# Performance work log

Measured on AMD Instinct MI355X. Metric: run time of the kernel, lower is better.

Reference implementation:

```python
import jax, jax.numpy as jnp
import numpy as np

PAD = 0
B, M, N, E = 32, 512, 512, 768
NEG_INF = 1e12
SCALE = np.float32(np.sqrt(768.0))


def submult(a, b):
    d = a - b
    return jnp.concatenate([a, b, d, a * b, d * d], axis=-1)


def setup_inputs() -> dict:
    key = jax.random.key(0)
    ks = jax.random.split(key, 8)
    c_ids = jax.random.randint(ks[0], (B, M), 1, 30000)
    c_ids = c_ids.at[:, 3 * M // 4 :].set(PAD)  # trailing padding
    r_ids = jax.random.randint(ks[1], (B, N), 1, 30000)
    r_ids = r_ids.at[:, 3 * N // 4 :].set(PAD)
    c_hs = jax.random.normal(ks[2], (B, M, E), dtype=jnp.float32)
    r_hs = jax.random.normal(ks[3], (B, N, E), dtype=jnp.float32)
    W_pre = jax.random.normal(ks[4], (5 * E, E), dtype=jnp.float32) * 0.02
    b_pre = jnp.zeros((E,), dtype=jnp.float32)
    W_ff1 = jax.random.normal(ks[5], (15 * E, E), dtype=jnp.float32) * 0.02
    b_ff1 = jnp.zeros((E,), dtype=jnp.float32)
    W_ff2 = jax.random.normal(ks[6], (E, 1), dtype=jnp.float32) * 0.02
    b_ff2 = jnp.zeros((1,), dtype=jnp.float32)
    return {
        "c_ids": c_ids, "r_ids": r_ids, "c_hs": c_hs, "r_hs": r_hs,
        "W_pre": W_pre, "b_pre": b_pre,
        "W_ff1": W_ff1, "b_ff1": b_ff1, "W_ff2": W_ff2, "b_ff2": b_ff2,
    }


def reference(c_ids, r_ids, c_hs, r_hs, W_pre, b_pre, W_ff1, b_ff1, W_ff2, b_ff2):
    cm = c_ids != PAD  # [B,M]
    rm = r_ids != PAD  # [B,N]
    # bidirectional cross-attention
    att = jnp.einsum("bme,bne->bmn", c_hs, r_hs) / SCALE
    pair_mask = cm[:, :, None] & rm[:, None, :]
    att = jnp.where(pair_mask, att, -NEG_INF)
    c_hat = jnp.einsum("bne,bmn->bme", r_hs, jax.nn.softmax(att, axis=-1))
    r_hat = jnp.einsum("bme,bmn->bne", c_hs, jax.nn.softmax(att, axis=-2))
    # submult expansion + pre_rnn (Linear + ReLU)
    c_bar = jax.nn.relu(submult(c_hat, c_hs) @ W_pre + b_pre)  # [B,M,E]
    r_bar = jax.nn.relu(submult(r_hat, r_hs) @ W_pre + b_pre)  # [B,N,E]
    # zero out padded positions
    c_x = jnp.where(cm[:, :, None], c_bar, 0.0)
    r_x = jnp.where(rm[:, :, None], r_bar, 0.0)
    c_cnt = cm.sum(-1).astype(c_x.dtype)[:, None]
    r_cnt = rm.sum(-1).astype(r_x.dtype)[:, None]
    c_feat = jnp.concatenate([c_x[:, 0], c_x.sum(1) / c_cnt, c_x.max(1)], axis=-1)
    r_feat = jnp.concatenate([r_x[:, 0], r_x.sum(1) / r_cnt, r_x.max(1)], axis=-1)
    m_vs = submult(c_feat, r_feat)  # [B, 15*E]
    h = jax.nn.relu(m_vs @ W_ff1 + b_ff1)
    scores = (h @ W_ff2 + b_ff2)[:, 0]  # [B]
    return scores
```

## Files before the change

### kernel.cpp

```cpp
#include <hip/hip_runtime.h>
#include <math.h>

#define B_ 32
#define M_ 512
#define N_ 512
#define E_ 768
#define NEG_BIG   -1e12f
#define INV_SCALE 0.03608439182435161f

typedef __attribute__((ext_vector_type(8))) __bf16 bf16x8;
typedef __attribute__((ext_vector_type(4))) float  floatx4;

#define MFMA_BF16 __builtin_amdgcn_mfma_f32_16x16x32_bf16

__device__ __forceinline__ void load16(const float* __restrict__ p, float* v) {
    *(float4*)&v[0]  = *(const float4*)(p);
    *(float4*)&v[4]  = *(const float4*)(p + 4);
    *(float4*)&v[8]  = *(const float4*)(p + 8);
    *(float4*)&v[12] = *(const float4*)(p + 12);
}

__device__ __forceinline__ void cvt_store16(const float* v, __bf16* hi, __bf16* lo,
                                            int row, int h) {
    bf16x8 h0, h1, l0, l1;
#pragma unroll
    for (int j = 0; j < 8; ++j) {
        float x0 = v[j], x1 = v[j + 8];
        __bf16 a0 = (__bf16)x0;
        __bf16 a1 = (__bf16)x1;
        h0[j] = a0;
        h1[j] = a1;
        l0[j] = (__bf16)(x0 - (float)a0);
        l1[j] = (__bf16)(x1 - (float)a1);
    }
    const int xr = (row >> 1) & 3;
    *(bf16x8*)&hi[row * 32 + (((2 * h)     ^ xr) << 3)] = h0;
    *(bf16x8*)&hi[row * 32 + (((2 * h + 1) ^ xr) << 3)] = h1;
    *(bf16x8*)&lo[row * 32 + (((2 * h)     ^ xr) << 3)] = l0;
    *(bf16x8*)&lo[row * 32 + (((2 * h + 1) ^ xr) << 3)] = l1;
}

__device__ __forceinline__ void mfma_step(const __bf16* Ahi, const __bf16* Alo,
                                          const __bf16* Bhi, const __bf16* Blo,
                                          const int (&aoff)[4], const int (&boff)[4],
                                          floatx4 (&acc)[4][4]) {
    bf16x8 bh[4], bl[4];
#pragma unroll
    for (int fn = 0; fn < 4; ++fn) {
        bh[fn] = *(const bf16x8*)&Bhi[boff[fn]];
        bl[fn] = *(const bf16x8*)&Blo[boff[fn]];
    }
#pragma unroll
    for (int fm = 0; fm < 4; ++fm) {
        bf16x8 ah = *(const bf16x8*)&Ahi[aoff[fm]];
        bf16x8 al = *(const bf16x8*)&Alo[aoff[fm]];
#pragma unroll
        for (int fn = 0; fn < 4; ++fn) {
            acc[fm][fn] = MFMA_BF16(ah, bh[fn], acc[fm][fn], 0, 0, 0);
            acc[fm][fn] = MFMA_BF16(ah, bl[fn], acc[fm][fn], 0, 0, 0);
            acc[fm][fn] = MFMA_BF16(al, bh[fn], acc[fm][fn], 0, 0, 0);
        }
    }
}

#define TILE_SETUP()                                                      \
    const int tid = threadIdx.x, lane = tid & 63;                         \
    const int l15 = lane & 15, l4 = lane >> 4;                            \
    const int wid = tid >> 6, wm = wid >> 1, wn = wid & 1;                \
    const int srow = tid >> 1, h = tid & 1;                               \
    int aoff[4], boff[4];                                                 \
    _Pragma("unroll")                                                     \
    for (int f = 0; f < 4; ++f) {                                         \
        int rr = wm * 64 + f * 16 + l15;                                  \
        aoff[f] = rr * 32 + ((l4 ^ ((rr >> 1) & 3)) << 3);                \
        int cc = wn * 64 + f * 16 + l15;                                  \
        boff[f] = cc * 32 + ((l4 ^ ((cc >> 1) & 3)) << 3);                \
    }                                                                     \
    floatx4 acc[4][4];                                                    \
    const floatx4 zero_ = {0.f, 0.f, 0.f, 0.f};                           \
    _Pragma("unroll")                                                     \
    for (int i = 0; i < 4; ++i)                                           \
        _Pragma("unroll")                                                 \
        for (int j = 0; j < 4; ++j) acc[i][j] = zero_;

__global__ __launch_bounds__(256, 2)
void mfma_att(const float* __restrict__ chs, const float* __restrict__ rhs,
              const int* __restrict__ cids, const int* __restrict__ rids,
              float* __restrict__ att) {
    __shared__ __bf16 Ahi[4096], Alo[4096], Bhi[4096], Blo[4096];
    const int b = blockIdx.z, m0 = blockIdx.x * 128, n0 = blockIdx.y * 128;
    TILE_SETUP();
    const float* Ap = chs + ((size_t)b * M_ + m0 + srow) * E_ + h * 16;
    const float* Bp = rhs + ((size_t)b * N_ + n0 + srow) * E_ + h * 16;

    for (int k0 = 0; k0 < E_; k0 += 32) {
        float va[16], vb[16];
        load16(Ap + k0, va);
        load16(Bp + k0, vb);
        __syncthreads();
        cvt_store16(va, Ahi, Alo, srow, h);
        cvt_store16(vb, Bhi, Blo, srow, h);
        __syncthreads();
        mfma_step(Ahi, Alo, Bhi, Blo, aoff, boff, acc);
    }

    bool rm[4];
#pragma unroll
    for (int fn = 0; fn < 4; ++fn)
        rm[fn] = rids[b * N_ + n0 + wn * 64 + fn * 16 + l15] != 0;
    float* Cb = att + (size_t)b * M_ * N_;
#pragma unroll
    for (int fm = 0; fm < 4; ++fm) {
        const int rbase = m0 + wm * 64 + fm * 16 + l4 * 4;
#pragma unroll
        for (int r = 0; r < 4; ++r) {
            const int row = rbase + r;
            const bool cm = cids[b * M_ + row] != 0;
#pragma unroll
            for (int fn = 0; fn < 4; ++fn) {
                float vv = (cm && rm[fn]) ? acc[fm][fn][r] * INV_SCALE : NEG_BIG;
                Cb[(size_t)row * N_ + n0 + wn * 64 + fn * 16 + l15] = vv;
            }
        }
    }
}

__global__ __launch_bounds__(256, 2)
void mfma_nn(const float* __restrict__ A, const float* __restrict__ Bg,
             float* __restrict__ C) {
    __shared__ __bf16 Ahi[4096], Alo[4096], Bhi[4096], Blo[4096];
    __shared__ float scr[32 * 132];
    const int b = blockIdx.z, m0 = blockIdx.x * 128, n0 = blockIdx.y * 128;
    TILE_SETUP();
    const float* Ap = A + ((size_t)b * M_ + m0 + srow) * 512 + h * 16;
    const float* Bbase = Bg + (size_t)b * 512 * E_ + n0;
    const int kk = tid >> 3, cseg = (tid & 7) * 16;

    for (int k0 = 0; k0 < 512; k0 += 32) {
        float va[16], wv[16];
        load16(Ap + k0, va);
        load16(Bbase + (size_t)(k0 + kk) * E_ + cseg, wv);
        __syncthreads();
        cvt_store16(va, Ahi, Alo, srow, h);
        *(float4*)&scr[kk * 132 + cseg]      = *(float4*)&wv[0];
        *(float4*)&scr[kk * 132 + cseg + 4]  = *(float4*)&wv[4];
        *(float4*)&scr[kk * 132 + cseg + 8]  = *(float4*)&wv[8];
        *(float4*)&scr[kk * 132 + cseg + 12] = *(float4*)&wv[12];
        __syncthreads();
        float vb[16];
#pragma unroll
        for (int j = 0; j < 16; ++j) vb[j] = scr[(h * 16 + j) * 132 + srow];
        cvt_store16(vb, Bhi, Blo, srow, h);
        __syncthreads();
        mfma_step(Ahi, Alo, Bhi, Blo, aoff, boff, acc);
    }

    float* Cb = C + (size_t)b * M_ * E_;
#pragma unroll
    for (int fm = 0; fm < 4; ++fm) {
        const int rbase = m0 + wm * 64 + fm * 16 + l4 * 4;
#pragma unroll
        for (int r = 0; r < 4; ++r)
#pragma unroll
            for (int fn = 0; fn < 4; ++fn)
                Cb[(size_t)(rbase + r) * E_ + n0 + wn * 64 + fn * 16 + l15] =
                    acc[fm][fn][r];
    }
}

__global__ __launch_bounds__(256, 2)
void mfma_feat(const float* __restrict__ HAT, const float* __restrict__ HS,
               const float* __restrict__ WT, const float* __restrict__ bias,
               const int* __restrict__ ids, float* __restrict__ stats) {
    __shared__ __bf16 Ahi[4096], Alo[4096], Bhi[4096], Blo[4096];
    const int m0 = blockIdx.x * 128, n0 = blockIdx.y * 128;
    TILE_SETUP();
    const float* Hp = HAT + (size_t)(m0 + srow) * E_ + h * 16;
    const float* Sp = HS + (size_t)(m0 + srow) * E_ + h * 16;
    const float* Wp = WT + (size_t)(n0 + srow) * 3840 + h * 16;

    for (int seg = 0; seg < 5; ++seg) {
        for (int e0 = 0; e0 < E_; e0 += 32) {
            float ha[16], sb[16], wv[16], f[16];
            load16(Hp + e0, ha);
            load16(Sp + e0, sb);
            load16(Wp + seg * E_ + e0, wv);
#pragma unroll
            for (int j = 0; j < 16; ++j) {
                float a = ha[j], bq = sb[j], d = a - bq;
                f[j] = (seg == 0) ? a : (seg == 1) ? bq : (seg == 2) ? d
                     : (seg == 3) ? a * bq : d * d;
            }
            __syncthreads();
            cvt_store16(f, Ahi, Alo, srow, h);
            cvt_store16(wv, Bhi, Blo, srow, h);
            __syncthreads();
            mfma_step(Ahi, Alo, Bhi, Blo, aoff, boff, acc);
        }
    }

    const int b = m0 >> 9;
    float bv[4];
#pragma unroll
    for (int fn = 0; fn < 4; ++fn)
        bv[fn] = bias[n0 + wn * 64 + fn * 16 + l15];
    float sum4[4] = {0.f, 0.f, 0.f, 0.f}, max4[4] = {0.f, 0.f, 0.f, 0.f};
#pragma unroll
    for (int fm = 0; fm < 4; ++fm) {
        const int rbase = m0 + wm * 64 + fm * 16 + l4 * 4;
#pragma unroll
        for (int r = 0; r < 4; ++r) {
            const int g = rbase + r;
            const bool valid = ids[g] != 0;
#pragma unroll
            for (int fn = 0; fn < 4; ++fn) {
                float v = fmaxf(acc[fm][fn][r] + bv[fn], 0.f);
                v = valid ? v : 0.f;
                sum4[fn] += v;
                max4[fn] = fmaxf(max4[fn], v);
                if ((g & 511) == 0)
                    stats[b * 2304 + n0 + wn * 64 + fn * 16 + l15] = v;
            }
        }
    }
#pragma unroll
    for (int fn = 0; fn < 4; ++fn) {
        float s = sum4[fn];
        s += __shfl_xor(s, 16); s += __shfl_xor(s, 32);
        float mx = max4[fn];
        mx = fmaxf(mx, __shfl_xor(mx, 16)); mx = fmaxf(mx, __shfl_xor(mx, 32));
        if (l4 == 0) {
            const int col = n0 + wn * 64 + fn * 16 + l15;
            atomicAdd(&stats[b * 2304 + 768 + col], s);
            atomicMax((int*)&stats[b * 2304 + 1536 + col], __float_as_int(mx));
        }
    }
}

__global__ __launch_bounds__(256)
void transpose_w(const float* __restrict__ src, float* __restrict__ dst) {
    __shared__ float tile[32][33];
    const int c0 = blockIdx.x * 32, r0 = blockIdx.y * 32;
    const int tx = threadIdx.x & 31, ty = threadIdx.x >> 5;
#pragma unroll
    for (int i = 0; i < 32; i += 8)
        tile[ty + i][tx] = src[(size_t)(r0 + ty + i) * 768 + c0 + tx];
    __syncthreads();
#pragma unroll
    for (int i = 0; i < 32; i += 8)
        dst[(size_t)(c0 + ty + i) * 3840 + r0 + tx] = tile[tx][ty + i];
}

__global__ __launch_bounds__(256)
void softmax_rows(const float* __restrict__ att, float* __restrict__ P) {
    const int wave = threadIdx.x >> 6;
    const int lane = threadIdx.x & 63;
    const size_t row = (size_t)blockIdx.x * 4 + wave;
    const float* x = att + row * N_;
    float v[8];
    float mx = -INFINITY;
#pragma unroll
    for (int i = 0; i < 8; ++i) { v[i] = x[lane + i * 64]; mx = fmaxf(mx, v[i]); }
#pragma unroll
    for (int off = 32; off; off >>= 1) mx = fmaxf(mx, __shfl_xor(mx, off));
    float s = 0.f;
#pragma unroll
    for (int i = 0; i < 8; ++i) { v[i] = __expf(v[i] - mx); s += v[i]; }
#pragma unroll
    for (int off = 32; off; off >>= 1) s += __shfl_xor(s, off);
    const float inv = 1.f / s;
    float* y = P + row * N_;
#pragma unroll
    for (int i = 0; i < 8; ++i) y[lane + i * 64] = v[i] * inv;
}

__global__ __launch_bounds__(256)
void softmax_cols_t(const float* __restrict__ att, float* __restrict__ P2t) {
    __shared__ float tile[512][17];
    __shared__ float red[16][16];
    __shared__ float invs[16];
    const int b = blockIdx.x, n0 = blockIdx.y * 16;
    const int tid = threadIdx.x;
    const int c = tid & 15, r = tid >> 4;
    const float* src = att + (size_t)b * M_ * N_ + n0;
#pragma unroll 4
    for (int i = 0; i < 32; ++i) {
        int m = r + i * 16;
        tile[m][c] = src[(size_t)m * N_ + c];
    }
    __syncthreads();
    float mx = -INFINITY;
    for (int m = r; m < 512; m += 16) mx = fmaxf(mx, tile[m][c]);
    red[r][c] = mx;
    __syncthreads();
    if (r == 0) {
        float m2 = red[0][c];
#pragma unroll
        for (int j = 1; j < 16; ++j) m2 = fmaxf(m2, red[j][c]);
        invs[c] = m2;
    }
    __syncthreads();
    const float cmx = invs[c];
    float s = 0.f;
    for (int m = r; m < 512; m += 16) {
        float e = __expf(tile[m][c] - cmx);
        tile[m][c] = e;
        s += e;
    }
    __syncthreads();
    red[r][c] = s;
    __syncthreads();
    if (r == 0) {
        float st = 0.f;
#pragma unroll
        for (int j = 0; j < 16; ++j) st += red[j][c];
        invs[c] = 1.f / st;
    }
    __syncthreads();
    float* dst = P2t + ((size_t)b * N_ + n0) * M_;
#pragma unroll 4
    for (int i = 0; i < 32; ++i) {
        int lin = tid + i * 256;
        int cc = lin >> 9;
        int m = lin & 511;
        dst[(size_t)cc * M_ + m] = tile[m][cc] * invs[cc];
    }
}

__global__ __launch_bounds__(256)
void ffprep_kernel(const float* __restrict__ sc, const float* __restrict__ sr,
                   const int* __restrict__ cids, const int* __restrict__ rids,
                   float* __restrict__ mv) {
    __shared__ int redc[4], redr[4];
    const int b = blockIdx.x, tid = threadIdx.x;
    int cc = 0, cr = 0;
    for (int m = tid; m < 512; m += 256) {
        cc += (cids[b * 512 + m] != 0);
        cr += (rids[b * 512 + m] != 0);
    }
#pragma unroll
    for (int off = 32; off; off >>= 1) {
        cc += __shfl_xor(cc, off);
        cr += __shfl_xor(cr, off);
    }
    if ((tid & 63) == 0) { redc[tid >> 6] = cc; redr[tid >> 6] = cr; }
    __syncthreads();
    const float invc = 1.f / (float)(redc[0] + redc[1] + redc[2] + redc[3]);
    const float invr = 1.f / (float)(redr[0] + redr[1] + redr[2] + redr[3]);
    const float* scb = sc + b * 2304;
    const float* srb = sr + b * 2304;
    float* mvb = mv + (size_t)b * 11520;
    for (int i = tid; i < 2304; i += 256) {
        float a = scb[i], r = srb[i];
        if (i >= 768 && i < 1536) { a *= invc; r *= invr; }
        float d = a - r;
        mvb[i]        = a;
        mvb[2304 + i] = r;
        mvb[4608 + i] = d;
        mvb[6912 + i] = a * r;
        mvb[9216 + i] = d * d;
    }
}

__global__ __launch_bounds__(256)
void ff1_kernel(const float* __restrict__ mv, const float* __restrict__ W1,
                float* __restrict__ hacc) {
    const int j = blockIdx.x * 256 + threadIdx.x;
    const int e0 = blockIdx.y * 720;
    float acc[32];
#pragma unroll
    for (int b = 0; b < 32; ++b) acc[b] = 0.f;
    for (int ec = 0; ec < 720; ec += 4) {
        const float w0 = W1[(size_t)(e0 + ec + 0) * 768 + j];
        const float w1 = W1[(size_t)(e0 + ec + 1) * 768 + j];
        const float w2 = W1[(size_t)(e0 + ec + 2) * 768 + j];
        const float w3 = W1[(size_t)(e0 + ec + 3) * 768 + j];
#pragma unroll
        for (int b = 0; b < 32; ++b) {
            const float* mp = mv + (size_t)b * 11520 + e0 + ec;
            float a = acc[b];
            a = fmaf(mp[0], w0, a);
            a = fmaf(mp[1], w1, a);
            a = fmaf(mp[2], w2, a);
            a = fmaf(mp[3], w3, a);
            acc[b] = a;
        }
    }
#pragma unroll
    for (int b = 0; b < 32; ++b) atomicAdd(&hacc[b * 768 + j], acc[b]);
}

__global__ __launch_bounds__(256)
void score_kernel(const float* __restrict__ hacc, const float* __restrict__ b1,
                  const float* __restrict__ W2, const float* __restrict__ b2,
                  float* __restrict__ out) {
    const int b = blockIdx.x, tid = threadIdx.x;
    float acc = 0.f;
    for (int j = tid; j < 768; j += 256)
        acc += fmaxf(hacc[b * 768 + j] + b1[j], 0.f) * W2[j];
#pragma unroll
    for (int off = 32; off; off >>= 1) acc += __shfl_xor(acc, off);
    __shared__ float red[4];
    if ((tid & 63) == 0) red[tid >> 6] = acc;
    __syncthreads();
    if (tid == 0) out[b] = red[0] + red[1] + red[2] + red[3] + b2[0];
}

extern "C" void kernel_launch(void* const* d_in, const int* in_sizes, int n_in,
                              void* d_out, int out_size, void* d_ws, size_t ws_size,
                              hipStream_t stream) {
    const int*   c_ids = (const int*)d_in[0];
    const int*   r_ids = (const int*)d_in[1];
    const float* c_hs  = (const float*)d_in[2];
    const float* r_hs  = (const float*)d_in[3];
    const float* W_pre = (const float*)d_in[4];
    const float* b_pre = (const float*)d_in[5];
    const float* W_ff1 = (const float*)d_in[6];
    const float* b_ff1 = (const float*)d_in[7];
    const float* W_ff2 = (const float*)d_in[8];
    const float* b_ff2 = (const float*)d_in[9];
    float* out = (float*)d_out;
    float* ws  = (float*)d_ws;

    const size_t ATT = (size_t)B_ * M_ * N_;
    const size_t CH  = (size_t)B_ * M_ * E_;

    float* att  = ws;
    float* P1   = ws + ATT;
    float* P2t  = ws + 2 * ATT;
    float* chat = ws + 3 * ATT;
    float* rhat = ws;
    float* WT   = ws + CH;
    float* sc   = ws + 15532032;
    float* sr   = sc + 73728;
    float* hacc = sr + 73728;
    float* mv   = hacc + 24576;

    mfma_att<<<dim3(4, 4, 32), 256, 0, stream>>>(c_hs, r_hs, c_ids, r_ids, att);
    softmax_rows  <<<dim3(B_ * M_ / 4), 256, 0, stream>>>(att, P1);
    softmax_cols_t<<<dim3(B_, 32), 256, 0, stream>>>(att, P2t);
    mfma_nn<<<dim3(4, 6, 32), 256, 0, stream>>>(P1, r_hs, chat);
    hipMemsetAsync(sc, 0, 172032 * sizeof(float), stream);
    transpose_w<<<dim3(24, 120), 256, 0, stream>>>(W_pre, WT);
    mfma_nn<<<dim3(4, 6, 32), 256, 0, stream>>>(P2t, c_hs, rhat);
    mfma_feat<<<dim3(128, 6), 256, 0, stream>>>(chat, c_hs, WT, b_pre, c_ids, sc);
    mfma_feat<<<dim3(128, 6), 256, 0, stream>>>(rhat, r_hs, WT, b_pre, r_ids, sr);
    ffprep_kernel<<<dim3(32), 256, 0, stream>>>(sc, sr, c_ids, r_ids, mv);
    ff1_kernel<<<dim3(3, 16), 256, 0, stream>>>(mv, W_ff1, hacc);
    score_kernel<<<dim3(32), 256, 0, stream>>>(hacc, b_ff1, W_ff2, b_ff2, out);
}
```

Baseline: 1.394 ms.

## Prefetch next k-tile in registers and pre-split operands to bf16 hi/lo

```diff
diff --git a/kernel.cpp b/kernel.cpp
--- a/kernel.cpp
+++ b/kernel.cpp
@@ -12,6 +12,9 @@
 typedef __attribute__((ext_vector_type(4))) float  floatx4;
 
 #define MFMA_BF16 __builtin_amdgcn_mfma_f32_16x16x32_bf16
+
+#define BAR() do { asm volatile("s_waitcnt lgkmcnt(0)" ::: "memory"); \
+                   __builtin_amdgcn_s_barrier(); } while (0)
 
 __device__ __forceinline__ void load16(const float* __restrict__ p, float* v) {
     *(float4*)&v[0]  = *(const float4*)(p);
@@ -38,6 +41,15 @@
     *(bf16x8*)&hi[row * 32 + (((2 * h + 1) ^ xr) << 3)] = h1;
     *(bf16x8*)&lo[row * 32 + (((2 * h)     ^ xr) << 3)] = l0;
     *(bf16x8*)&lo[row * 32 + (((2 * h + 1) ^ xr) << 3)] = l1;
+}
+
+__device__ __forceinline__ void store_pre16(const bf16x8* v, __bf16* hi, __bf16* lo,
+                                            int row, int h) {
+    const int xr = (row >> 1) & 3;
+    *(bf16x8*)&hi[row * 32 + (((2 * h)     ^ xr) << 3)] = v[0];
+    *(bf16x8*)&hi[row * 32 + (((2 * h + 1) ^ xr) << 3)] = v[1];
+    *(bf16x8*)&lo[row * 32 + (((2 * h)     ^ xr) << 3)] = v[2];
+    *(bf16x8*)&lo[row * 32 + (((2 * h + 1) ^ xr) << 3)] = v[3];
 }
 
 __device__ __forceinline__ void mfma_step(const __bf16* Ahi, const __bf16* Alo,
@@ -93,14 +105,22 @@
     const float* Ap = chs + ((size_t)b * M_ + m0 + srow) * E_ + h * 16;
     const float* Bp = rhs + ((size_t)b * N_ + n0 + srow) * E_ + h * 16;
 
-    for (int k0 = 0; k0 < E_; k0 += 32) {
-        float va[16], vb[16];
-        load16(Ap + k0, va);
-        load16(Bp + k0, vb);
-        __syncthreads();
+    float va[16], vb[16], na[16], nb[16];
+    load16(Ap, va); load16(Bp, vb);
+#pragma unroll 1
+    for (int k0 = 0; k0 < E_; k0 += 64) {
+        BAR();
         cvt_store16(va, Ahi, Alo, srow, h);
         cvt_store16(vb, Bhi, Blo, srow, h);
-        __syncthreads();
+        load16(Ap + k0 + 32, na);
+        load16(Bp + k0 + 32, nb);
+        BAR();
+        mfma_step(Ahi, Alo, Bhi, Blo, aoff, boff, acc);
+        BAR();
+        cvt_store16(na, Ahi, Alo, srow, h);
+        cvt_store16(nb, Bhi, Blo, srow, h);
+        if (k0 + 64 < E_) { load16(Ap + k0 + 64, va); load16(Bp + k0 + 64, vb); }
+        BAR();
         mfma_step(Ahi, Alo, Bhi, Blo, aoff, boff, acc);
     }
 
@@ -126,32 +146,65 @@
 }
 
 __global__ __launch_bounds__(256, 2)
-void mfma_nn(const float* __restrict__ A, const float* __restrict__ Bg,
-             float* __restrict__ C) {
+void mfma_nn(const __bf16* __restrict__ Phi, const __bf16* __restrict__ Plo,
+             const float* __restrict__ Bg, float* __restrict__ C) {
     __shared__ __bf16 Ahi[4096], Alo[4096], Bhi[4096], Blo[4096];
     __shared__ float scr[32 * 132];
     const int b = blockIdx.z, m0 = blockIdx.x * 128, n0 = blockIdx.y * 128;
     TILE_SETUP();
-    const float* Ap = A + ((size_t)b * M_ + m0 + srow) * 512 + h * 16;
-    const float* Bbase = Bg + (size_t)b * 512 * E_ + n0;
+    const __bf16* Aph = Phi + ((size_t)b * 512 + m0 + srow) * 512 + h * 16;
+    const __bf16* Apl = Plo + ((size_t)b * 512 + m0 + srow) * 512 + h * 16;
     const int kk = tid >> 3, cseg = (tid & 7) * 16;
-
-    for (int k0 = 0; k0 < 512; k0 += 32) {
-        float va[16], wv[16];
-        load16(Ap + k0, va);
-        load16(Bbase + (size_t)(k0 + kk) * E_ + cseg, wv);
-        __syncthreads();
-        cvt_store16(va, Ahi, Alo, srow, h);
-        *(float4*)&scr[kk * 132 + cseg]      = *(float4*)&wv[0];
-        *(float4*)&scr[kk * 132 + cseg + 4]  = *(float4*)&wv[4];
-        *(float4*)&scr[kk * 132 + cseg + 8]  = *(float4*)&wv[8];
-        *(float4*)&scr[kk * 132 + cseg + 12] = *(float4*)&wv[12];
-        __syncthreads();
-        float vb[16];
-#pragma unroll
-        for (int j = 0; j < 16; ++j) vb[j] = scr[(h * 16 + j) * 132 + srow];
-        cvt_store16(vb, Bhi, Blo, srow, h);
-        __syncthreads();
+    const float* Bp = Bg + ((size_t)b * 512 + kk) * E_ + n0 + cseg;
+
+    bf16x8 a0[4], a1[4];
+    float w0[16], w1[16];
+    a0[0] = *(const bf16x8*)(Aph);     a0[1] = *(const bf16x8*)(Aph + 8);
+    a0[2] = *(const bf16x8*)(Apl);     a0[3] = *(const bf16x8*)(Apl + 8);
+    load16(Bp, w0);
+#pragma unroll 1
+    for (int k0 = 0; k0 < 512; k0 += 64) {
+        BAR();
+        store_pre16(a0, Ahi, Alo, srow, h);
+        *(float4*)&scr[kk * 132 + cseg]      = *(float4*)&w0[0];
+        *(float4*)&scr[kk * 132 + cseg + 4]  = *(float4*)&w0[4];
+        *(float4*)&scr[kk * 132 + cseg + 8]  = *(float4*)&w0[8];
+        *(float4*)&scr[kk * 132 + cseg + 12] = *(float4*)&w0[12];
+        a1[0] = *(const bf16x8*)(Aph + k0 + 32);
+        a1[1] = *(const bf16x8*)(Aph + k0 + 40);
+        a1[2] = *(const bf16x8*)(Apl + k0 + 32);
+        a1[3] = *(const bf16x8*)(Apl + k0 + 40);
+        load16(Bp + (size_t)(k0 + 32) * E_, w1);
+        BAR();
+        {
+            float vb16[16];
+#pragma unroll
+            for (int j = 0; j < 16; ++j) vb16[j] = scr[(h * 16 + j) * 132 + srow];
+            cvt_store16(vb16, Bhi, Blo, srow, h);
+        }
+        BAR();
+        mfma_step(Ahi, Alo, Bhi, Blo, aoff, boff, acc);
+        BAR();
+        store_pre16(a1, Ahi, Alo, srow, h);
+        *(float4*)&scr[kk * 132 + cseg]      = *(float4*)&w1[0];
+        *(float4*)&scr[kk * 132 + cseg + 4]  = *(float4*)&w1[4];
+        *(float4*)&scr[kk * 132 + cseg + 8]  = *(float4*)&w1[8];
+        *(float4*)&scr[kk * 132 + cseg + 12] = *(float4*)&w1[12];
+        if (k0 + 64 < 512) {
+            a0[0] = *(const bf16x8*)(Aph + k0 + 64);
+            a0[1] = *(const bf16x8*)(Aph + k0 + 72);
+            a0[2] = *(const bf16x8*)(Apl + k0 + 64);
+            a0[3] = *(const bf16x8*)(Apl + k0 + 72);
+            load16(Bp + (size_t)(k0 + 64) * E_, w0);
+        }
+        BAR();
+        {
+            float vb16[16];
+#pragma unroll
+            for (int j = 0; j < 16; ++j) vb16[j] = scr[(h * 16 + j) * 132 + srow];
+            cvt_store16(vb16, Bhi, Blo, srow, h);
+        }
+        BAR();
         mfma_step(Ahi, Alo, Bhi, Blo, aoff, boff, acc);
     }
 
@@ -168,33 +221,86 @@
     }
 }
 
+__device__ __forceinline__ void feature16(float* f, const float* a, const float* s,
+                                          int seg) {
+    if (seg == 0) {
+#pragma unroll
+        for (int j = 0; j < 16; ++j) f[j] = a[j];
+    } else if (seg == 1) {
+#pragma unroll
+        for (int j = 0; j < 16; ++j) f[j] = s[j];
+    } else if (seg == 2) {
+#pragma unroll
+        for (int j = 0; j < 16; ++j) f[j] = a[j] - s[j];
+    } else if (seg == 3) {
+#pragma unroll
+        for (int j = 0; j < 16; ++j) f[j] = a[j] * s[j];
+    } else {
+#pragma unroll
+        for (int j = 0; j < 16; ++j) { float d = a[j] - s[j]; f[j] = d * d; }
+    }
+}
+
 __global__ __launch_bounds__(256, 2)
-void mfma_feat(const float* __restrict__ HAT, const float* __restrict__ HS,
-               const float* __restrict__ WT, const float* __restrict__ bias,
-               const int* __restrict__ ids, float* __restrict__ stats) {
+void mfma_feat(const float* __restrict__ chat, const float* __restrict__ rhat,
+               const float* __restrict__ chs, const float* __restrict__ rhs,
+               const __bf16* __restrict__ WThi, const __bf16* __restrict__ WTlo,
+               const float* __restrict__ bias, const int* __restrict__ cids,
+               const int* __restrict__ rids, float* __restrict__ scs,
+               float* __restrict__ srs) {
     __shared__ __bf16 Ahi[4096], Alo[4096], Bhi[4096], Blo[4096];
+    const int side = blockIdx.z;
+    const float* HAT = side ? rhat : chat;
+    const float* HS  = side ? rhs  : chs;
+    const int*   ids = side ? rids : cids;
+    float*     stats = side ? srs  : scs;
     const int m0 = blockIdx.x * 128, n0 = blockIdx.y * 128;
     TILE_SETUP();
     const float* Hp = HAT + (size_t)(m0 + srow) * E_ + h * 16;
-    const float* Sp = HS + (size_t)(m0 + srow) * E_ + h * 16;
-    const float* Wp = WT + (size_t)(n0 + srow) * 3840 + h * 16;
-
-    for (int seg = 0; seg < 5; ++seg) {
-        for (int e0 = 0; e0 < E_; e0 += 32) {
-            float ha[16], sb[16], wv[16], f[16];
-            load16(Hp + e0, ha);
-            load16(Sp + e0, sb);
-            load16(Wp + seg * E_ + e0, wv);
-#pragma unroll
-            for (int j = 0; j < 16; ++j) {
-                float a = ha[j], bq = sb[j], d = a - bq;
-                f[j] = (seg == 0) ? a : (seg == 1) ? bq : (seg == 2) ? d
-                     : (seg == 3) ? a * bq : d * d;
+    const float* Sp = HS  + (size_t)(m0 + srow) * E_ + h * 16;
+    const __bf16* Wph = WThi + (size_t)(n0 + srow) * 3840 + h * 16;
+    const __bf16* Wpl = WTlo + (size_t)(n0 + srow) * 3840 + h * 16;
+
+    float a0v[16], s0v[16], a1v[16], s1v[16];
+    bf16x8 w0[4], w1[4];
+    load16(Hp, a0v); load16(Sp, s0v);
+    w0[0] = *(const bf16x8*)(Wph);     w0[1] = *(const bf16x8*)(Wph + 8);
+    w0[2] = *(const bf16x8*)(Wpl);     w0[3] = *(const bf16x8*)(Wpl + 8);
+
+#pragma unroll 1
+    for (int t = 0; t < 120; t += 2) {
+        {
+            float f[16];
+            feature16(f, a0v, s0v, t / 24);
+            BAR();
+            cvt_store16(f, Ahi, Alo, srow, h);
+            store_pre16(w0, Bhi, Blo, srow, h);
+            const int t1 = t + 1;
+            const int e1 = (t1 % 24) * 32;
+            load16(Hp + e1, a1v); load16(Sp + e1, s1v);
+            w1[0] = *(const bf16x8*)(Wph + t1 * 32);
+            w1[1] = *(const bf16x8*)(Wph + t1 * 32 + 8);
+            w1[2] = *(const bf16x8*)(Wpl + t1 * 32);
+            w1[3] = *(const bf16x8*)(Wpl + t1 * 32 + 8);
+            BAR();
+            mfma_step(Ahi, Alo, Bhi, Blo, aoff, boff, acc);
+        }
+        {
+            float f[16];
+            feature16(f, a1v, s1v, (t + 1) / 24);
+            BAR();
+            cvt_store16(f, Ahi, Alo, srow, h);
+            store_pre16(w1, Bhi, Blo, srow, h);
+            if (t + 2 < 120) {
+                const int t2 = t + 2;
+                const int e2 = (t2 % 24) * 32;
+                load16(Hp + e2, a0v); load16(Sp + e2, s0v);
+                w0[0] = *(const bf16x8*)(Wph + t2 * 32);
+                w0[1] = *(const bf16x8*)(Wph + t2 * 32 + 8);
+                w0[2] = *(const bf16x8*)(Wpl + t2 * 32);
+                w0[3] = *(const bf16x8*)(Wpl + t2 * 32 + 8);
             }
-            __syncthreads();
-            cvt_store16(f, Ahi, Alo, srow, h);
-            cvt_store16(wv, Bhi, Blo, srow, h);
-            __syncthreads();
+            BAR();
             mfma_step(Ahi, Alo, Bhi, Blo, aoff, boff, acc);
         }
     }
@@ -238,21 +344,29 @@
 }
 
 __global__ __launch_bounds__(256)
-void transpose_w(const float* __restrict__ src, float* __restrict__ dst) {
+void split_w(const float* __restrict__ src, __bf16* __restrict__ whi,
+             __bf16* __restrict__ wlo) {
     __shared__ float tile[32][33];
-    const int c0 = blockIdx.x * 32, r0 = blockIdx.y * 32;
+    const int c0 = blockIdx.x * 32;
+    const int r0 = blockIdx.y * 32;
     const int tx = threadIdx.x & 31, ty = threadIdx.x >> 5;
 #pragma unroll
     for (int i = 0; i < 32; i += 8)
         tile[ty + i][tx] = src[(size_t)(r0 + ty + i) * 768 + c0 + tx];
     __syncthreads();
-#pragma unroll
-    for (int i = 0; i < 32; i += 8)
-        dst[(size_t)(c0 + ty + i) * 3840 + r0 + tx] = tile[tx][ty + i];
+    const int nr = threadIdx.x >> 3, kq = (threadIdx.x & 7) * 4;
+#pragma unroll
+    for (int j = 0; j < 4; ++j) {
+        float v = tile[kq + j][nr];
+        __bf16 hv = (__bf16)v;
+        whi[(size_t)(c0 + nr) * 3840 + r0 + kq + j] = hv;
+        wlo[(size_t)(c0 + nr) * 3840 + r0 + kq + j] = (__bf16)(v - (float)hv);
+    }
 }
 
 __global__ __launch_bounds__(256)
-void softmax_rows(const float* __restrict__ att, float* __restrict__ P) {
+void softmax_rows(const float* __restrict__ att, __bf16* __restrict__ phi,
+                  __bf16* __restrict__ plo) {
     const int wave = threadIdx.x >> 6;
     const int lane = threadIdx.x & 63;
     const size_t row = (size_t)blockIdx.x * 4 + wave;
@@ -269,13 +383,18 @@
 #pragma unroll
     for (int off = 32; off; off >>= 1) s += __shfl_xor(s, off);
     const float inv = 1.f / s;
-    float* y = P + row * N_;
-#pragma unroll
-    for (int i = 0; i < 8; ++i) y[lane + i * 64] = v[i] * inv;
+#pragma unroll
+    for (int i = 0; i < 8; ++i) {
+        float val = v[i] * inv;
+        __bf16 hv = (__bf16)val;
+        phi[row * N_ + lane + i * 64] = hv;
+        plo[row * N_ + lane + i * 64] = (__bf16)(val - (float)hv);
+    }
 }
 
 __global__ __launch_bounds__(256)
-void softmax_cols_t(const float* __restrict__ att, float* __restrict__ P2t) {
+void softmax_cols_t(const float* __restrict__ att, __bf16* __restrict__ dhi,
+                    __bf16* __restrict__ dlo) {
     __shared__ float tile[512][17];
     __shared__ float red[16][16];
     __shared__ float invs[16];
@@ -317,13 +436,16 @@
         invs[c] = 1.f / st;
     }
     __syncthreads();
-    float* dst = P2t + ((size_t)b * N_ + n0) * M_;
 #pragma unroll 4
     for (int i = 0; i < 32; ++i) {
         int lin = tid + i * 256;
         int cc = lin >> 9;
         int m = lin & 511;
-        dst[(size_t)cc * M_ + m] = tile[m][cc] * invs[cc];
+        float val = tile[m][cc] * invs[cc];
+        __bf16 hv = (__bf16)val;
+        const size_t o = ((size_t)b * N_ + n0 + cc) * M_ + m;
+        dhi[o] = hv;
+        dlo[o] = (__bf16)(val - (float)hv);
     }
 }
 
@@ -422,29 +544,30 @@
     float* out = (float*)d_out;
     float* ws  = (float*)d_ws;
 
-    const size_t ATT = (size_t)B_ * M_ * N_;
-    const size_t CH  = (size_t)B_ * M_ * E_;
-
-    float* att  = ws;
-    float* P1   = ws + ATT;
-    float* P2t  = ws + 2 * ATT;
-    float* chat = ws + 3 * ATT;
-    float* rhat = ws;
-    float* WT   = ws + CH;
-    float* sc   = ws + 15532032;
-    float* sr   = sc + 73728;
-    float* hacc = sr + 73728;
-    float* mv   = hacc + 24576;
+    float* att   = ws;
+    __bf16* P1hi  = (__bf16*)(ws + 8388608);
+    __bf16* P1lo  = (__bf16*)(ws + 12582912);
+    __bf16* P2thi = (__bf16*)(ws + 16777216);
+    __bf16* P2tlo = (__bf16*)(ws + 20971520);
+    float* chat  = ws + 25165824;
+    float* rhat  = ws;
+    __bf16* WThi  = (__bf16*)(ws + 12582912);
+    __bf16* WTlo  = (__bf16*)(ws + 14057472);
+    float* sc    = ws + 15532032;
+    float* sr    = sc + 73728;
+    float* hacc  = sr + 73728;
+    float* mv    = hacc + 24576;
 
     mfma_att<<<dim3(4, 4, 32), 256, 0, stream>>>(c_hs, r_hs, c_ids, r_ids, att);
-    softmax_rows  <<<dim3(B_ * M_ / 4), 256, 0, stream>>>(att, P1);
-    softmax_cols_t<<<dim3(B_, 32), 256, 0, stream>>>(att, P2t);
-    mfma_nn<<<dim3(4, 6, 32), 256, 0, stream>>>(P1, r_hs, chat);
+    softmax_rows  <<<dim3(B_ * M_ / 4), 256, 0, stream>>>(att, P1hi, P1lo);
+    softmax_cols_t<<<dim3(B_, 32), 256, 0, stream>>>(att, P2thi, P2tlo);
+    mfma_nn<<<dim3(4, 6, 32), 256, 0, stream>>>(P1hi, P1lo, r_hs, chat);
+    split_w<<<dim3(24, 120), 256, 0, stream>>>(W_pre, WThi, WTlo);
     hipMemsetAsync(sc, 0, 172032 * sizeof(float), stream);
-    transpose_w<<<dim3(24, 120), 256, 0, stream>>>(W_pre, WT);
-    mfma_nn<<<dim3(4, 6, 32), 256, 0, stream>>>(P2t, c_hs, rhat);
-    mfma_feat<<<dim3(128, 6), 256, 0, stream>>>(chat, c_hs, WT, b_pre, c_ids, sc);
-    mfma_feat<<<dim3(128, 6), 256, 0, stream>>>(rhat, r_hs, WT, b_pre, r_ids, sr);
+    mfma_nn<<<dim3(4, 6, 32), 256, 0, stream>>>(P2thi, P2tlo, c_hs, rhat);
+    mfma_feat<<<dim3(128, 6, 2), 256, 0, stream>>>(chat, rhat, c_hs, r_hs,
+                                                   WThi, WTlo, b_pre,
+                                                   c_ids, r_ids, sc, sr);
     ffprep_kernel<<<dim3(32), 256, 0, stream>>>(sc, sr, c_ids, r_ids, mv);
     ff1_kernel<<<dim3(3, 16), 256, 0, stream>>>(mv, W_ff1, hacc);
     score_kernel<<<dim3(32), 256, 0, stream>>>(hacc, b_ff1, W_ff2, b_ff2, out);
```

Result: slower. 1.519 ms (+8.9%).
